# Kernel optimization log

Hardware: AMD Instinct MI355X
Metric: run time of the kernel (lower is better)

## Reference

```python
import jax, jax.numpy as jnp
import numpy as np

NUM_CLASSES = 80
CONF_THRESH = 0.05
NMS_THRESH = 0.6
TOPK = 1000
LEVEL_HWS = [40000, 10000, 2500, 640, 160]
CLASS_OFFSET = 2.0  # > max box coordinate so different classes never overlap (class-aware NMS)


def setup_inputs() -> dict:
    key = jax.random.key(0)
    inp = {}
    for i, hw in enumerate(LEVEL_HWS):
        k1, k2, k3, key = jax.random.split(key, 4)
        inp[f"cls_p{i + 3}"] = jax.random.normal(k1, (1, hw, NUM_CLASSES), jnp.float32)
        inp[f"ctn_p{i + 3}"] = jax.random.normal(k2, (1, hw, 1), jnp.float32)
        inp[f"box_p{i + 3}"] = jax.random.uniform(k3, (1, hw, 4), jnp.float32)
    inp["img_size"] = 1600
    return inp


def _level_select(cls_p, ctn_p, box_p):
    # cls_p: [1, HW, C], ctn_p: [1, HW, 1], box_p: [1, HW, 4]
    cls_p, ctn_p, box_p = cls_p[0], ctn_p[0], box_p[0]
    k = min(TOPK, box_p.shape[0])  # matches min(self.topk, box_pred_i.size(0))
    scores = jnp.sqrt(jax.nn.sigmoid(cls_p) * jax.nn.sigmoid(ctn_p)).reshape(-1)  # [HW*C]
    topk_scores, topk_idxs = jax.lax.top_k(scores, k)  # descending, == sort+slice
    valid = topk_scores > CONF_THRESH  # mask instead of dynamic filter (jit-friendly)
    labels = topk_idxs % NUM_CLASSES
    anchor_idxs = topk_idxs // NUM_CLASSES
    return topk_scores * valid, labels, box_p[anchor_idxs], valid


def _pairwise_iou(boxes):
    # boxes: [N, 4] xyxy
    x1, y1, x2, y2 = boxes[:, 0], boxes[:, 1], boxes[:, 2], boxes[:, 3]
    area = jnp.maximum(x2 - x1, 0.0) * jnp.maximum(y2 - y1, 0.0)
    ix1 = jnp.maximum(x1[:, None], x1[None, :])
    iy1 = jnp.maximum(y1[:, None], y1[None, :])
    ix2 = jnp.minimum(x2[:, None], x2[None, :])
    iy2 = jnp.minimum(y2[:, None], y2[None, :])
    inter = jnp.maximum(ix2 - ix1, 0.0) * jnp.maximum(iy2 - iy1, 0.0)
    union = area[:, None] + area[None, :] - inter
    return inter / jnp.maximum(union, 1e-9)


def _greedy_nms(scores, boxes, valid, thresh):
    # exact greedy NMS over a fixed-size candidate set; returns keep mask [N]
    n = scores.shape[0]
    order = jnp.argsort(-scores)
    iou = _pairwise_iou(boxes[order])  # [N, N]
    idx = jnp.arange(n)

    def body(i, keep):
        sup = (iou[i] > thresh) & keep[i] & (idx > i)
        return keep & (~sup)

    keep_o = jax.lax.fori_loop(0, n, body, valid[order])
    return jnp.zeros(n, dtype=bool).at[order].set(keep_o)


def reference(cls_p3, ctn_p3, box_p3, cls_p4, ctn_p4, box_p4,
              cls_p5, ctn_p5, box_p5, cls_p6, ctn_p6, box_p6,
              cls_p7, ctn_p7, box_p7, img_size):
    levels = [(cls_p3, ctn_p3, box_p3), (cls_p4, ctn_p4, box_p4),
              (cls_p5, ctn_p5, box_p5), (cls_p6, ctn_p6, box_p6),
              (cls_p7, ctn_p7, box_p7)]
    parts = [_level_select(c, t, b) for (c, t, b) in levels]
    scores = jnp.concatenate([p[0] for p in parts])   # [3800]
    labels = jnp.concatenate([p[1] for p in parts])   # [3800] int
    bboxes = jnp.concatenate([p[2] for p in parts])   # [3800, 4]
    valid = jnp.concatenate([p[3] for p in parts])    # [3800] bool
    # class-aware multiclass NMS via coordinate offset per class
    boxes_off = bboxes + (labels.astype(bboxes.dtype) * CLASS_OFFSET)[:, None]
    keep = _greedy_nms(jax.lax.stop_gradient(scores),
                       jax.lax.stop_gradient(boxes_off), valid, NMS_THRESH)
    # normalize to [0,1] by image size (square image: W == H == img_size)
    bboxes_n = jnp.clip(bboxes / jnp.float32(img_size), 0.0, 1.0)
    return scores * keep, labels, bboxes_n, keep
```

## Files before the change

kernel.cpp:

```cpp
#include <hip/hip_runtime.h>
#include <math.h>

#pragma clang fp contract(off)

typedef unsigned long long ull;

#define NCLS 80
#define NTOT 3800
#define CAND_CAP 4096
#define NMS_CAP 1024
#define CLS_CAP 128
#define BIN_LO 0x3F000000u
#define NB 1024
#define BSHIFT 13
#define QPB 1024
#define NBLK 1044
#define SEGCAP 320
#define ZWORDS 6496

__constant__ int d_BSQ[6]  = {0, 782, 978, 1027, 1040, 1044};
__constant__ int d_QL[5]   = {800000, 200000, 50000, 12800, 3200};
__constant__ int d_EL[5]   = {3200000, 800000, 200000, 51200, 12800};
__constant__ float d_PREHI[5] = {0.86f, 0.82f, 0.78f, 0.74f, 0.74f};
__constant__ int d_KL[5] = {1000,1000,1000,640,160};
__constant__ int d_OB[5] = {0,1000,2000,3000,3640};

struct Params {
  const float *cls0,*cls1,*cls2,*cls3,*cls4;
  const float *ctn0,*ctn1,*ctn2,*ctn3,*ctn4;
  const float *box0,*box1,*box2,*box3,*box4;
  const int* img;
  ull* pre;
  unsigned* tot;
  unsigned* ccount;
  unsigned* clscnt;
  unsigned* lvlbad;
  unsigned* blkcnt;
  ull* ckey;
  ull* clskey;
  unsigned* slot_bits;
  unsigned* slot_label;
  float* slot_box;
  float* out;
};

__device__ __forceinline__ float fast_sig(float x) {
  return 1.0f / (1.0f + __expf(-x));
}
__device__ __forceinline__ float fast_score(float c, float t) {
  return sqrtf(fast_sig(c) * fast_sig(t));
}
__device__ __forceinline__ float sigmoid_ref(float x) {
  float e = (float)exp(-(double)x);
  return 1.0f / (1.0f + e);
}
__device__ __forceinline__ float score_ref(float c, float t) {
  return sqrtf(sigmoid_ref(c) * sigmoid_ref(t));
}
__device__ __forceinline__ float iou_ref(float ax1,float ay1,float ax2,float ay2,
                                         float bx1,float by1,float bx2,float by2) {
  float areaA = fmaxf(ax2-ax1,0.0f) * fmaxf(ay2-ay1,0.0f);
  float areaB = fmaxf(bx2-bx1,0.0f) * fmaxf(by2-by1,0.0f);
  float ix1 = fmaxf(ax1,bx1), iy1 = fmaxf(ay1,by1);
  float ix2 = fminf(ax2,bx2), iy2 = fminf(ay2,by2);
  float inter = fmaxf(ix2-ix1,0.0f) * fmaxf(iy2-iy1,0.0f);
  float uni = areaA + areaB - inter;
  return inter / fmaxf(uni, 1e-9f);
}
__device__ __forceinline__ const float* cls_of(const Params& p, int l) {
  return (l==0)?p.cls0:(l==1)?p.cls1:(l==2)?p.cls2:(l==3)?p.cls3:p.cls4;
}
__device__ __forceinline__ const float* ctn_of(const Params& p, int l) {
  return (l==0)?p.ctn0:(l==1)?p.ctn1:(l==2)?p.ctn2:(l==3)?p.ctn3:p.ctn4;
}
__device__ __forceinline__ const float* box_of(const Params& p, int l) {
  return (l==0)?p.box0:(l==1)?p.box1:(l==2)?p.box2:(l==3)?p.box3:p.box4;
}

__global__ __launch_bounds__(256) void k_zero(unsigned* z) {
  for (int i = blockIdx.x*256 + threadIdx.x; i < ZWORDS; i += 256) z[i] = 0u;
}

__global__ __launch_bounds__(256) void k_score(Params p) {
  int b = blockIdx.x, tid = threadIdx.x;
  __shared__ unsigned h[NB];
  __shared__ ull pbuf[SEGCAP];
  __shared__ unsigned pcnt;
  for (int i = tid; i < NB; i += 256) h[i] = 0u;
  if (tid == 0) pcnt = 0u;
  __syncthreads();
  int l = 0;
  while (b >= d_BSQ[l+1]) ++l;
  int cb = b - d_BSQ[l];
  int q0 = cb * QPB;
  int nq = d_QL[l] - q0; if (nq > QPB) nq = QPB;
  const float* cls = cls_of(p, l);
  const float* ctn = ctn_of(p, l);
  float prehi = d_PREHI[l];
  for (int i = tid; i < nq; i += 256) {
    int q = q0 + i;
    float4 c4 = ((const float4*)cls)[q];
    float st = fast_sig(ctn[q / 20]);
    float s[4];
    s[0] = sqrtf(fast_sig(c4.x) * st);
    s[1] = sqrtf(fast_sig(c4.y) * st);
    s[2] = sqrtf(fast_sig(c4.z) * st);
    s[3] = sqrtf(fast_sig(c4.w) * st);
    #pragma unroll
    for (int j = 0; j < 4; ++j) {
      unsigned bits = __float_as_uint(s[j]);
      if (bits >= BIN_LO) atomicAdd(&h[(bits - BIN_LO) >> BSHIFT], 1u);
      if (s[j] >= prehi) {
        unsigned pos = atomicAdd(&pcnt, 1u);
        if (pos < SEGCAP)
          pbuf[pos] = ((ull)bits << 32) | (ull)(0xFFFFFFFFu - (unsigned)(4*q + j));
      }
    }
  }
  __syncthreads();
  unsigned* tl = p.tot + l*NB;
  for (int i = tid; i < NB; i += 256) {
    unsigned v = h[i];
    if (v) atomicAdd(&tl[i], v);
  }
  unsigned n = pcnt;
  if (tid == 0) {
    p.blkcnt[b] = n;
    if (n > SEGCAP) p.lvlbad[l] = 1u;
  }
  unsigned nw = n < SEGCAP ? n : SEGCAP;
  ull* seg = p.pre + (size_t)b * SEGCAP;
  for (unsigned i = tid; i < nw; i += 256) seg[i] = pbuf[i];
}

__global__ __launch_bounds__(256) void k_gather(Params p) {
  int bx = blockIdx.x;
  int l = bx >> 3, slice = bx & 7;
  int tid = threadIdx.x;
  __shared__ unsigned sfx[NB];
  __shared__ ull cbuf[CAND_CAP];
  __shared__ unsigned pcnt;
  __shared__ unsigned thr_sh;
  __shared__ unsigned base_sh;
  if (tid == 0) { pcnt = 0u; thr_sh = BIN_LO; }
  for (int j = tid; j < NB; j += 256) sfx[j] = p.tot[l*NB + j];
  __syncthreads();
  for (int off = 1; off < NB; off <<= 1) {
    unsigned v[4];
    #pragma unroll
    for (int j = 0; j < 4; ++j) {
      int idx = tid + j*256;
      unsigned add = (idx + off < NB) ? sfx[idx + off] : 0u;
      v[j] = sfx[idx] + add;
    }
    __syncthreads();
    #pragma unroll
    for (int j = 0; j < 4; ++j) sfx[tid + j*256] = v[j];
    __syncthreads();
  }
  unsigned k = (unsigned)d_KL[l];
  #pragma unroll
  for (int j = 0; j < 4; ++j) {
    int b = tid + j*256;
    unsigned s0 = sfx[b];
    unsigned s1 = (b + 1 < NB) ? sfx[b+1] : 0u;
    if (s0 >= k && (b == NB-1 || s1 < k)) {
      thr_sh = (b > 0) ? (BIN_LO + ((unsigned)(b-1) << BSHIFT)) : BIN_LO;
    }
  }
  __syncthreads();
  unsigned thr = thr_sh;
  const float* cls = cls_of(p, l);
  const float* ctn = ctn_of(p, l);
  bool fallback = (p.lvlbad[l] != 0u) || (thr < __float_as_uint(d_PREHI[l]));
  if (!fallback) {
    int s0b = d_BSQ[l], nseg = d_BSQ[l+1] - s0b;
    int chunk = (nseg + 7) >> 3;
    int sA = slice * chunk, sB = sA + chunk;
    if (sA > nseg) sA = nseg;
    if (sB > nseg) sB = nseg;
    int total = (sB - sA) * SEGCAP;
    const ull* base = p.pre + (size_t)(s0b + sA) * SEGCAP;
    const unsigned* bc = p.blkcnt + s0b + sA;
    for (int i = tid; i < total; i += 256) {
      int s = i / SEGCAP;
      int j = i - s * SEGCAP;
      unsigned cnt = bc[s]; if (cnt > SEGCAP) cnt = SEGCAP;
      if (j < (int)cnt) {
        ull kk = base[(size_t)s * SEGCAP + j];
        if ((unsigned)(kk >> 32) >= thr) {
          unsigned fi = 0xFFFFFFFFu - (unsigned)kk;
          float ex = score_ref(cls[fi], ctn[fi / NCLS]);
          unsigned pos = atomicAdd(&pcnt, 1u);
          if (pos < CAND_CAP)
            cbuf[pos] = ((ull)__float_as_uint(ex) << 32) | (ull)(0xFFFFFFFFu - fi);
        }
      }
    }
  } else {
    int ne = d_EL[l];
    int chunk = (ne + 7) >> 3;
    int eA = slice * chunk, eB = eA + chunk;
    if (eA > ne) eA = ne;
    if (eB > ne) eB = ne;
    for (int e = eA + tid; e < eB; e += 256) {
      float s = fast_score(cls[e], ctn[e / NCLS]);
      if (__float_as_uint(s) >= thr) {
        float ex = score_ref(cls[e], ctn[e / NCLS]);
        unsigned pos = atomicAdd(&pcnt, 1u);
        if (pos < CAND_CAP)
          cbuf[pos] = ((ull)__float_as_uint(ex) << 32) | (ull)(0xFFFFFFFFu - (unsigned)e);
      }
    }
  }
  __syncthreads();
  unsigned n = pcnt; if (n > CAND_CAP) n = CAND_CAP;
  if (tid == 0) base_sh = atomicAdd(&p.ccount[l*16], n);
  __syncthreads();
  unsigned bp = base_sh;
  ull* ck = p.ckey + (size_t)l * CAND_CAP;
  for (unsigned i = tid; i < n; i += 256) {
    unsigned d = bp + i;
    if (d < CAND_CAP) ck[d] = cbuf[i];
  }
}

__global__ __launch_bounds__(64) void k_rank(Params p) {
  int bx = blockIdx.x;
  int l = bx >> 6, slice = bx & 63;
  int tid = threadIdx.x;
  int m = (int)p.ccount[l*16]; if (m > CAND_CAP) m = CAND_CAP;
  int kL = d_KL[l], obase = d_OB[l];
  int i0 = slice * 64;
  int i = i0 + tid;
  if (i0 >= m) {
    if (i >= m && i < kL) {
      int g = obase + i;
      p.out[g] = 0.0f;
      p.out[NTOT + g] = 0.0f;
      ((float4*)(p.out + 2*NTOT))[g] = make_float4(0,0,0,0);
      p.out[6*NTOT + g] = 0.0f;
      ((float4*)p.slot_box)[g] = make_float4(0,0,0,0);
      p.slot_bits[g] = 0u;
      p.slot_label[g] = 0xFFFFFFFFu;
    }
    return;
  }
  __shared__ ull key[CAND_CAP];
  const ull* ck = p.ckey + (size_t)l * CAND_CAP;
  for (int j = tid; j < m; j += 64) key[j] = ck[j];
  __syncthreads();
  if (i >= m) {
    if (i < kL) {
      int g = obase + i;
      p.out[g] = 0.0f;
      p.out[NTOT + g] = 0.0f;
      ((float4*)(p.out + 2*NTOT))[g] = make_float4(0,0,0,0);
      p.out[6*NTOT + g] = 0.0f;
      ((float4*)p.slot_box)[g] = make_float4(0,0,0,0);
      p.slot_bits[g] = 0u;
      p.slot_label[g] = 0xFFFFFFFFu;
    }
    return;
  }
  ull mine = key[i];
  int rank = 0;
  int mm = m & ~7;
  #pragma unroll 1
  for (int j = 0; j < mm; j += 8) {
    rank += (key[j  ] > mine) + (key[j+1] > mine) + (key[j+2] > mine) + (key[j+3] > mine)
          + (key[j+4] > mine) + (key[j+5] > mine) + (key[j+6] > mine) + (key[j+7] > mine);
  }
  for (int j = mm; j < m; ++j) rank += (key[j] > mine) ? 1 : 0;
  if (rank >= kL) return;
  int g = obase + rank;
  unsigned bits = (unsigned)(mine >> 32);
  unsigned fi = 0xFFFFFFFFu - (unsigned)(mine & 0xFFFFFFFFu);
  unsigned lab = fi % NCLS;
  unsigned a = fi / NCLS;
  float img = (float)(*p.img);
  float4 b4 = ((const float4*)box_of(p, l))[a];
  float4 nb;
  nb.x = fminf(fmaxf(b4.x / img, 0.0f), 1.0f);
  nb.y = fminf(fmaxf(b4.y / img, 0.0f), 1.0f);
  nb.z = fminf(fmaxf(b4.z / img, 0.0f), 1.0f);
  nb.w = fminf(fmaxf(b4.w / img, 0.0f), 1.0f);
  p.out[NTOT + g] = (float)lab;
  ((float4*)(p.out + 2*NTOT))[g] = nb;
  ((float4*)p.slot_box)[g] = b4;
  p.slot_bits[g] = bits;
  p.slot_label[g] = lab;
  unsigned pos = atomicAdd(&p.clscnt[lab*16], 1u);
  if (pos < CLS_CAP)
    p.clskey[lab*CLS_CAP + pos] = ((ull)bits << 32) | (ull)(0xFFFFFFFFu - (unsigned)g);
}

__global__ __launch_bounds__(64) void k_nms(Params p) {
  int c = blockIdx.x, lane = threadIdx.x;
  int mc = (int)p.clscnt[c*16];
  if (mc == 0) return;
  if (mc <= 64) {
    ull kk = (lane < mc) ? p.clskey[c*CLS_CAP + lane] : 0ULL;
    int rank = 0;
    #pragma unroll 1
    for (int j = 0; j < 64; ++j) {
      ull kj = __shfl(kk, j);
      rank += (j < mc && kj > kk) ? 1 : 0;
    }
    __shared__ ull wkey[64];
    if (lane < mc) wkey[rank] = kk;
    __syncthreads();
    ull sk = (lane < mc) ? wkey[lane] : 0ULL;
    unsigned g = 0xFFFFFFFFu - (unsigned)(sk & 0xFFFFFFFFu);
    float s = __uint_as_float((unsigned)(sk >> 32));
    float off = 2.0f * (float)c;
    float x1=0,y1=0,x2=0,y2=0;
    if (lane < mc) {
      float4 b4 = ((const float4*)p.slot_box)[g];
      x1 = b4.x + off; y1 = b4.y + off; x2 = b4.z + off; y2 = b4.w + off;
    }
    ull keepm = __ballot(lane < mc && s > 0.05f);
    for (int i = 0; i + 1 < mc; ++i) {
      if ((keepm >> i) & 1ULL) {
        float ax1 = __shfl(x1, i), ay1 = __shfl(y1, i);
        float ax2 = __shfl(x2, i), ay2 = __shfl(y2, i);
        bool kept = (keepm >> lane) & 1ULL;
        bool sup = kept && (lane > i) && (lane < mc) &&
                   (iou_ref(ax1,ay1,ax2,ay2, x1,y1,x2,y2) > 0.6f);
        keepm &= ~__ballot(sup);
      }
    }
    if (lane < mc) {
      int kp = (int)((keepm >> lane) & 1ULL);
      p.out[g] = kp ? s : 0.0f;
      p.out[6*NTOT + g] = kp ? 1.0f : 0.0f;
    }
    return;
  }
  __shared__ ull key[NMS_CAP];
  __shared__ ull skey[NMS_CAP];
  __shared__ float bxs[NMS_CAP*4];
  __shared__ int keep[NMS_CAP];
  __shared__ unsigned mcnt_s;
  int m;
  if (mc <= CLS_CAP) {
    for (int j = lane; j < mc; j += 64) key[j] = p.clskey[c*CLS_CAP + j];
    m = mc;
    __syncthreads();
  } else {
    if (lane == 0) mcnt_s = 0u;
    __syncthreads();
    for (int g = lane; g < NTOT; g += 64) {
      if (p.slot_label[g] == (unsigned)c) {
        unsigned pos = atomicAdd(&mcnt_s, 1u);
        if (pos < NMS_CAP)
          key[pos] = ((ull)p.slot_bits[g] << 32) | (ull)(0xFFFFFFFFu - (unsigned)g);
      }
    }
    __syncthreads();
    m = (mcnt_s < NMS_CAP) ? (int)mcnt_s : NMS_CAP;
  }
  for (int i = lane; i < m; i += 64) {
    ull mine = key[i];
    int rank = 0;
    for (int j = 0; j < m; ++j) rank += (key[j] > mine) ? 1 : 0;
    skey[rank] = mine;
  }
  __syncthreads();
  float off = 2.0f * (float)c;
  for (int j = lane; j < m; j += 64) {
    ull kk = skey[j];
    unsigned g = 0xFFFFFFFFu - (unsigned)(kk & 0xFFFFFFFFu);
    for (int q = 0; q < 4; ++q) bxs[j*4+q] = p.slot_box[g*4+q] + off;
    float s = __uint_as_float((unsigned)(kk >> 32));
    keep[j] = (s > 0.05f) ? 1 : 0;
  }
  __syncthreads();
  for (int i = 0; i + 1 < m; ++i) {
    if (keep[i]) {
      float ax1 = bxs[i*4+0], ay1 = bxs[i*4+1], ax2 = bxs[i*4+2], ay2 = bxs[i*4+3];
      for (int j = i + 1 + lane; j < m; j += 64) {
        if (keep[j]) {
          if (iou_ref(ax1,ay1,ax2,ay2, bxs[j*4+0],bxs[j*4+1],bxs[j*4+2],bxs[j*4+3]) > 0.6f)
            keep[j] = 0;
        }
      }
    }
    __syncthreads();
  }
  for (int j = lane; j < m; j += 64) {
    ull kk = skey[j];
    unsigned g = 0xFFFFFFFFu - (unsigned)(kk & 0xFFFFFFFFu);
    float s = __uint_as_float((unsigned)(kk >> 32));
    int kp = keep[j];
    p.out[g] = kp ? s : 0.0f;
    p.out[6*NTOT + g] = kp ? 1.0f : 0.0f;
  }
}

extern "C" void kernel_launch(void* const* d_in, const int* in_sizes, int n_in,
                              void* d_out, int out_size, void* d_ws, size_t ws_size,
                              hipStream_t stream) {
  Params p;
  p.cls0 = (const float*)d_in[0];  p.ctn0 = (const float*)d_in[1];  p.box0 = (const float*)d_in[2];
  p.cls1 = (const float*)d_in[3];  p.ctn1 = (const float*)d_in[4];  p.box1 = (const float*)d_in[5];
  p.cls2 = (const float*)d_in[6];  p.ctn2 = (const float*)d_in[7];  p.box2 = (const float*)d_in[8];
  p.cls3 = (const float*)d_in[9];  p.ctn3 = (const float*)d_in[10]; p.box3 = (const float*)d_in[11];
  p.cls4 = (const float*)d_in[12]; p.ctn4 = (const float*)d_in[13]; p.box4 = (const float*)d_in[14];
  p.img  = (const int*)d_in[15];

  char* w = (char*)d_ws;
  p.pre = (ull*)w;            w += (size_t)NBLK*SEGCAP*8;
  unsigned* zbase = (unsigned*)w;
  p.tot    = zbase;
  p.ccount = zbase + 5120;
  p.clscnt = zbase + 5120 + 80;
  p.lvlbad = zbase + 5120 + 80 + 1280;
  w += (size_t)ZWORDS*4;
  p.blkcnt = (unsigned*)w;    w += (size_t)NBLK*4 + 64;
  p.ckey = (ull*)w;           w += (size_t)5*CAND_CAP*8;
  p.clskey = (ull*)w;         w += (size_t)NCLS*CLS_CAP*8;
  p.slot_bits  = (unsigned*)w; w += NTOT*4;
  p.slot_label = (unsigned*)w; w += NTOT*4;
  p.slot_box   = (float*)w;    w += NTOT*16;
  p.out = (float*)d_out;

  hipLaunchKernelGGL(k_zero,   dim3(1),     dim3(256), 0, stream, zbase);
  hipLaunchKernelGGL(k_score,  dim3(NBLK),  dim3(256), 0, stream, p);
  hipLaunchKernelGGL(k_gather, dim3(40),    dim3(256), 0, stream, p);
  hipLaunchKernelGGL(k_rank,   dim3(5*64),  dim3(64),  0, stream, p);
  hipLaunchKernelGGL(k_nms,    dim3(80),    dim3(64),  0, stream, p);
}
```

Baseline: 209.5 us.

## Fuse gather into score and rank kernels, compacting candidates globally

```diff
diff --git a/kernel.cpp b/kernel.cpp
--- a/kernel.cpp
+++ b/kernel.cpp
@@ -15,7 +15,8 @@
 #define BSHIFT 13
 #define QPB 1024
 #define NBLK 1044
-#define SEGCAP 320
+#define PBUF_CAP 320
+#define GCAP 16384
 #define ZWORDS 6496
 
 __constant__ int d_BSQ[6]  = {0, 782, 978, 1027, 1040, 1044};
@@ -30,13 +31,11 @@
   const float *ctn0,*ctn1,*ctn2,*ctn3,*ctn4;
   const float *box0,*box1,*box2,*box3,*box4;
   const int* img;
-  ull* pre;
   unsigned* tot;
-  unsigned* ccount;
+  unsigned* gcnt;
   unsigned* clscnt;
   unsigned* lvlbad;
-  unsigned* blkcnt;
-  ull* ckey;
+  ull* gcand;
   ull* clskey;
   unsigned* slot_bits;
   unsigned* slot_label;
@@ -83,10 +82,9 @@
 
 __global__ __launch_bounds__(256) void k_score(Params p) {
   int b = blockIdx.x, tid = threadIdx.x;
-  __shared__ unsigned h[NB];
-  __shared__ ull pbuf[SEGCAP];
+  __shared__ ull pbuf[PBUF_CAP];
   __shared__ unsigned pcnt;
-  for (int i = tid; i < NB; i += 256) h[i] = 0u;
+  __shared__ unsigned base_sh;
   if (tid == 0) pcnt = 0u;
   __syncthreads();
   int l = 0;
@@ -97,159 +95,122 @@
   const float* cls = cls_of(p, l);
   const float* ctn = ctn_of(p, l);
   float prehi = d_PREHI[l];
+  unsigned* tl = p.tot + l*NB;
   for (int i = tid; i < nq; i += 256) {
     int q = q0 + i;
     float4 c4 = ((const float4*)cls)[q];
-    float st = fast_sig(ctn[q / 20]);
-    float s[4];
-    s[0] = sqrtf(fast_sig(c4.x) * st);
-    s[1] = sqrtf(fast_sig(c4.y) * st);
-    s[2] = sqrtf(fast_sig(c4.z) * st);
-    s[3] = sqrtf(fast_sig(c4.w) * st);
+    float ct = ctn[q / 20];
+    float st = fast_sig(ct);
+    float cv[4] = {c4.x, c4.y, c4.z, c4.w};
     #pragma unroll
     for (int j = 0; j < 4; ++j) {
-      unsigned bits = __float_as_uint(s[j]);
-      if (bits >= BIN_LO) atomicAdd(&h[(bits - BIN_LO) >> BSHIFT], 1u);
-      if (s[j] >= prehi) {
+      float s = sqrtf(fast_sig(cv[j]) * st);
+      if (s >= prehi) {
+        unsigned fb = __float_as_uint(s);
+        unsigned bin = (fb - BIN_LO) >> BSHIFT;
+        if (bin > NB-1) bin = NB-1;
+        atomicAdd(&tl[bin], 1u);
+        float ex = score_ref(cv[j], ct);
         unsigned pos = atomicAdd(&pcnt, 1u);
-        if (pos < SEGCAP)
-          pbuf[pos] = ((ull)bits << 32) | (ull)(0xFFFFFFFFu - (unsigned)(4*q + j));
-      }
-    }
-  }
-  __syncthreads();
-  unsigned* tl = p.tot + l*NB;
-  for (int i = tid; i < NB; i += 256) {
-    unsigned v = h[i];
-    if (v) atomicAdd(&tl[i], v);
-  }
+        if (pos < PBUF_CAP)
+          pbuf[pos] = ((ull)__float_as_uint(ex) << 32)
+                    | (ull)(0xFFFFFFFFu - (unsigned)(4*q + j));
+      }
+    }
+  }
+  __syncthreads();
   unsigned n = pcnt;
-  if (tid == 0) {
-    p.blkcnt[b] = n;
-    if (n > SEGCAP) p.lvlbad[l] = 1u;
-  }
-  unsigned nw = n < SEGCAP ? n : SEGCAP;
-  ull* seg = p.pre + (size_t)b * SEGCAP;
-  for (unsigned i = tid; i < nw; i += 256) seg[i] = pbuf[i];
-}
-
-__global__ __launch_bounds__(256) void k_gather(Params p) {
-  int bx = blockIdx.x;
-  int l = bx >> 3, slice = bx & 7;
-  int tid = threadIdx.x;
-  __shared__ unsigned sfx[NB];
-  __shared__ ull cbuf[CAND_CAP];
-  __shared__ unsigned pcnt;
-  __shared__ unsigned thr_sh;
-  __shared__ unsigned base_sh;
-  if (tid == 0) { pcnt = 0u; thr_sh = BIN_LO; }
-  for (int j = tid; j < NB; j += 256) sfx[j] = p.tot[l*NB + j];
-  __syncthreads();
-  for (int off = 1; off < NB; off <<= 1) {
-    unsigned v[4];
-    #pragma unroll
-    for (int j = 0; j < 4; ++j) {
-      int idx = tid + j*256;
-      unsigned add = (idx + off < NB) ? sfx[idx + off] : 0u;
-      v[j] = sfx[idx] + add;
-    }
-    __syncthreads();
-    #pragma unroll
-    for (int j = 0; j < 4; ++j) sfx[tid + j*256] = v[j];
-    __syncthreads();
-  }
-  unsigned k = (unsigned)d_KL[l];
-  #pragma unroll
-  for (int j = 0; j < 4; ++j) {
-    int b = tid + j*256;
-    unsigned s0 = sfx[b];
-    unsigned s1 = (b + 1 < NB) ? sfx[b+1] : 0u;
-    if (s0 >= k && (b == NB-1 || s1 < k)) {
-      thr_sh = (b > 0) ? (BIN_LO + ((unsigned)(b-1) << BSHIFT)) : BIN_LO;
-    }
-  }
-  __syncthreads();
-  unsigned thr = thr_sh;
-  const float* cls = cls_of(p, l);
-  const float* ctn = ctn_of(p, l);
-  bool fallback = (p.lvlbad[l] != 0u) || (thr < __float_as_uint(d_PREHI[l]));
-  if (!fallback) {
-    int s0b = d_BSQ[l], nseg = d_BSQ[l+1] - s0b;
-    int chunk = (nseg + 7) >> 3;
-    int sA = slice * chunk, sB = sA + chunk;
-    if (sA > nseg) sA = nseg;
-    if (sB > nseg) sB = nseg;
-    int total = (sB - sA) * SEGCAP;
-    const ull* base = p.pre + (size_t)(s0b + sA) * SEGCAP;
-    const unsigned* bc = p.blkcnt + s0b + sA;
-    for (int i = tid; i < total; i += 256) {
-      int s = i / SEGCAP;
-      int j = i - s * SEGCAP;
-      unsigned cnt = bc[s]; if (cnt > SEGCAP) cnt = SEGCAP;
-      if (j < (int)cnt) {
-        ull kk = base[(size_t)s * SEGCAP + j];
-        if ((unsigned)(kk >> 32) >= thr) {
-          unsigned fi = 0xFFFFFFFFu - (unsigned)kk;
-          float ex = score_ref(cls[fi], ctn[fi / NCLS]);
-          unsigned pos = atomicAdd(&pcnt, 1u);
-          if (pos < CAND_CAP)
-            cbuf[pos] = ((ull)__float_as_uint(ex) << 32) | (ull)(0xFFFFFFFFu - fi);
-        }
-      }
-    }
-  } else {
-    int ne = d_EL[l];
-    int chunk = (ne + 7) >> 3;
-    int eA = slice * chunk, eB = eA + chunk;
-    if (eA > ne) eA = ne;
-    if (eB > ne) eB = ne;
-    for (int e = eA + tid; e < eB; e += 256) {
-      float s = fast_score(cls[e], ctn[e / NCLS]);
-      if (__float_as_uint(s) >= thr) {
-        float ex = score_ref(cls[e], ctn[e / NCLS]);
-        unsigned pos = atomicAdd(&pcnt, 1u);
-        if (pos < CAND_CAP)
-          cbuf[pos] = ((ull)__float_as_uint(ex) << 32) | (ull)(0xFFFFFFFFu - (unsigned)e);
-      }
-    }
-  }
-  __syncthreads();
-  unsigned n = pcnt; if (n > CAND_CAP) n = CAND_CAP;
-  if (tid == 0) base_sh = atomicAdd(&p.ccount[l*16], n);
-  __syncthreads();
-  unsigned bp = base_sh;
-  ull* ck = p.ckey + (size_t)l * CAND_CAP;
+  if (n > PBUF_CAP) { if (tid == 0) p.lvlbad[l] = 1u; n = PBUF_CAP; }
+  if (tid == 0) base_sh = atomicAdd(&p.gcnt[l*16], n);
+  __syncthreads();
+  unsigned base = base_sh;
+  ull* gc = p.gcand + (size_t)l * GCAP;
   for (unsigned i = tid; i < n; i += 256) {
-    unsigned d = bp + i;
-    if (d < CAND_CAP) ck[d] = cbuf[i];
+    unsigned d = base + i;
+    if (d < GCAP) gc[d] = pbuf[i];
+    else p.lvlbad[l] = 1u;
   }
 }
 
 __global__ __launch_bounds__(64) void k_rank(Params p) {
   int bx = blockIdx.x;
   int l = bx >> 6, slice = bx & 63;
-  int tid = threadIdx.x;
-  int m = (int)p.ccount[l*16]; if (m > CAND_CAP) m = CAND_CAP;
+  int lane = threadIdx.x;
+  __shared__ unsigned hist[NB];
+  __shared__ ull key[CAND_CAP];
+  for (int j = 0; j < NB/64; ++j)
+    hist[lane + j*64] = p.tot[l*NB + lane + j*64];
+  __syncthreads();
+  int chunkbase = 1008 - 16*lane;
+  unsigned csum = 0;
+  #pragma unroll
+  for (int t = 0; t < 16; ++t) csum += hist[chunkbase + t];
+  unsigned cum = csum;
+  for (int d = 1; d < 64; d <<= 1) {
+    unsigned tu = __shfl_up(cum, d);
+    if (lane >= d) cum += tu;
+  }
+  unsigned k = (unsigned)d_KL[l];
+  ull okm = __ballot(cum >= k);
+  unsigned thr = BIN_LO;
+  if (okm) {
+    int j0 = (int)__ffsll((long long)okm) - 1;
+    if (lane == j0) {
+      unsigned acc = cum - csum;
+      int cb2 = 1008 - 16*j0;
+      for (int bb = cb2 + 15; bb >= cb2; --bb) {
+        acc += hist[bb];
+        if (acc >= k) {
+          if (bb > 0) thr = BIN_LO + ((unsigned)(bb - 1) << BSHIFT);
+          break;
+        }
+      }
+    }
+    thr = __shfl(thr, j0);
+  }
+  bool fastok = (p.lvlbad[l] == 0u) && (thr >= __float_as_uint(d_PREHI[l]));
+  int m = 0;
+  if (fastok) {
+    int gn = (int)p.gcnt[l*16]; if (gn > GCAP) gn = GCAP;
+    const ull* gc = p.gcand + (size_t)l * GCAP;
+    for (int i0 = 0; i0 < gn; i0 += 64) {
+      int i = i0 + lane;
+      ull kk = (i < gn) ? gc[i] : 0ULL;
+      bool pred = (i < gn) && ((unsigned)(kk >> 32) >= thr);
+      ull mask = __ballot(pred);
+      if (pred) {
+        int pos = m + (int)__popcll(mask & ((1ULL << lane) - 1ULL));
+        if (pos < CAND_CAP) key[pos] = kk;
+      }
+      m += (int)__popcll(mask);
+    }
+  } else {
+    int ne = d_EL[l];
+    const float* cls = cls_of(p, l);
+    const float* ctn = ctn_of(p, l);
+    for (int i0 = 0; i0 < ne; i0 += 64) {
+      int i = i0 + lane;
+      bool pred = false; ull kk = 0ULL;
+      if (i < ne) {
+        float fs = fast_score(cls[i], ctn[i / NCLS]);
+        if (__float_as_uint(fs) >= thr) {
+          float ex = score_ref(cls[i], ctn[i / NCLS]);
+          kk = ((ull)__float_as_uint(ex) << 32) | (ull)(0xFFFFFFFFu - (unsigned)i);
+          pred = true;
+        }
+      }
+      ull mask = __ballot(pred);
+      if (pred) {
+        int pos = m + (int)__popcll(mask & ((1ULL << lane) - 1ULL));
+        if (pos < CAND_CAP) key[pos] = kk;
+      }
+      m += (int)__popcll(mask);
+    }
+  }
+  if (m > CAND_CAP) m = CAND_CAP;
+  __syncthreads();
   int kL = d_KL[l], obase = d_OB[l];
-  int i0 = slice * 64;
-  int i = i0 + tid;
-  if (i0 >= m) {
-    if (i >= m && i < kL) {
-      int g = obase + i;
-      p.out[g] = 0.0f;
-      p.out[NTOT + g] = 0.0f;
-      ((float4*)(p.out + 2*NTOT))[g] = make_float4(0,0,0,0);
-      p.out[6*NTOT + g] = 0.0f;
-      ((float4*)p.slot_box)[g] = make_float4(0,0,0,0);
-      p.slot_bits[g] = 0u;
-      p.slot_label[g] = 0xFFFFFFFFu;
-    }
-    return;
-  }
-  __shared__ ull key[CAND_CAP];
-  const ull* ck = p.ckey + (size_t)l * CAND_CAP;
-  for (int j = tid; j < m; j += 64) key[j] = ck[j];
-  __syncthreads();
+  int i = slice*64 + lane;
   if (i >= m) {
     if (i < kL) {
       int g = obase + i;
@@ -410,24 +371,21 @@
   p.img  = (const int*)d_in[15];
 
   char* w = (char*)d_ws;
-  p.pre = (ull*)w;            w += (size_t)NBLK*SEGCAP*8;
   unsigned* zbase = (unsigned*)w;
   p.tot    = zbase;
-  p.ccount = zbase + 5120;
+  p.gcnt   = zbase + 5120;
   p.clscnt = zbase + 5120 + 80;
   p.lvlbad = zbase + 5120 + 80 + 1280;
   w += (size_t)ZWORDS*4;
-  p.blkcnt = (unsigned*)w;    w += (size_t)NBLK*4 + 64;
-  p.ckey = (ull*)w;           w += (size_t)5*CAND_CAP*8;
-  p.clskey = (ull*)w;         w += (size_t)NCLS*CLS_CAP*8;
+  p.gcand = (ull*)w;           w += (size_t)5*GCAP*8;
+  p.clskey = (ull*)w;          w += (size_t)NCLS*CLS_CAP*8;
   p.slot_bits  = (unsigned*)w; w += NTOT*4;
   p.slot_label = (unsigned*)w; w += NTOT*4;
   p.slot_box   = (float*)w;    w += NTOT*16;
   p.out = (float*)d_out;
 
-  hipLaunchKernelGGL(k_zero,   dim3(1),     dim3(256), 0, stream, zbase);
-  hipLaunchKernelGGL(k_score,  dim3(NBLK),  dim3(256), 0, stream, p);
-  hipLaunchKernelGGL(k_gather, dim3(40),    dim3(256), 0, stream, p);
-  hipLaunchKernelGGL(k_rank,   dim3(5*64),  dim3(64),  0, stream, p);
-  hipLaunchKernelGGL(k_nms,    dim3(80),    dim3(64),  0, stream, p);
-}
+  hipLaunchKernelGGL(k_zero,  dim3(1),    dim3(256), 0, stream, zbase);
+  hipLaunchKernelGGL(k_score, dim3(NBLK), dim3(256), 0, stream, p);
+  hipLaunchKernelGGL(k_rank,  dim3(5*64), dim3(64),  0, stream, p);
+  hipLaunchKernelGGL(k_nms,   dim3(80),   dim3(64),  0, stream, p);
+}
```

Measured after the change: 527.0 us. 152% more time.

## Compact pre-candidates globally and compute exact scores in the scoring kernel

Applied to the files above, without the earlier changes.

```diff
diff --git a/kernel.cpp b/kernel.cpp
--- a/kernel.cpp
+++ b/kernel.cpp
@@ -15,8 +15,9 @@
 #define BSHIFT 13
 #define QPB 1024
 #define NBLK 1044
-#define SEGCAP 320
-#define ZWORDS 6496
+#define PBUF_CAP 320
+#define GCAP 65536
+#define ZWORDS 6576
 
 __constant__ int d_BSQ[6]  = {0, 782, 978, 1027, 1040, 1044};
 __constant__ int d_QL[5]   = {800000, 200000, 50000, 12800, 3200};
@@ -30,12 +31,12 @@
   const float *ctn0,*ctn1,*ctn2,*ctn3,*ctn4;
   const float *box0,*box1,*box2,*box3,*box4;
   const int* img;
-  ull* pre;
   unsigned* tot;
+  unsigned* gcnt;
   unsigned* ccount;
   unsigned* clscnt;
   unsigned* lvlbad;
-  unsigned* blkcnt;
+  ull* gcand;
   ull* ckey;
   ull* clskey;
   unsigned* slot_bits;
@@ -83,10 +84,9 @@
 
 __global__ __launch_bounds__(256) void k_score(Params p) {
   int b = blockIdx.x, tid = threadIdx.x;
-  __shared__ unsigned h[NB];
-  __shared__ ull pbuf[SEGCAP];
+  __shared__ ull pbuf[PBUF_CAP];
   __shared__ unsigned pcnt;
-  for (int i = tid; i < NB; i += 256) h[i] = 0u;
+  __shared__ unsigned base_sh;
   if (tid == 0) pcnt = 0u;
   __syncthreads();
   int l = 0;
@@ -97,43 +97,44 @@
   const float* cls = cls_of(p, l);
   const float* ctn = ctn_of(p, l);
   float prehi = d_PREHI[l];
+  unsigned* tl = p.tot + l*NB;
   for (int i = tid; i < nq; i += 256) {
     int q = q0 + i;
     float4 c4 = ((const float4*)cls)[q];
-    float st = fast_sig(ctn[q / 20]);
-    float s[4];
-    s[0] = sqrtf(fast_sig(c4.x) * st);
-    s[1] = sqrtf(fast_sig(c4.y) * st);
-    s[2] = sqrtf(fast_sig(c4.z) * st);
-    s[3] = sqrtf(fast_sig(c4.w) * st);
+    float ct = ctn[q / 20];
+    float st = fast_sig(ct);
+    float cv[4] = {c4.x, c4.y, c4.z, c4.w};
     #pragma unroll
     for (int j = 0; j < 4; ++j) {
-      unsigned bits = __float_as_uint(s[j]);
-      if (bits >= BIN_LO) atomicAdd(&h[(bits - BIN_LO) >> BSHIFT], 1u);
-      if (s[j] >= prehi) {
+      float s = sqrtf(fast_sig(cv[j]) * st);
+      if (s >= prehi) {
+        unsigned fb = __float_as_uint(s);
+        unsigned bin = (fb - BIN_LO) >> BSHIFT;
+        if (bin > NB-1) bin = NB-1;
+        atomicAdd(&tl[bin], 1u);
+        float ex = score_ref(cv[j], ct);
         unsigned pos = atomicAdd(&pcnt, 1u);
-        if (pos < SEGCAP)
-          pbuf[pos] = ((ull)bits << 32) | (ull)(0xFFFFFFFFu - (unsigned)(4*q + j));
-      }
-    }
-  }
-  __syncthreads();
-  unsigned* tl = p.tot + l*NB;
-  for (int i = tid; i < NB; i += 256) {
-    unsigned v = h[i];
-    if (v) atomicAdd(&tl[i], v);
-  }
+        if (pos < PBUF_CAP)
+          pbuf[pos] = ((ull)__float_as_uint(ex) << 32)
+                    | (ull)(0xFFFFFFFFu - (unsigned)(4*q + j));
+      }
+    }
+  }
+  __syncthreads();
   unsigned n = pcnt;
-  if (tid == 0) {
-    p.blkcnt[b] = n;
-    if (n > SEGCAP) p.lvlbad[l] = 1u;
-  }
-  unsigned nw = n < SEGCAP ? n : SEGCAP;
-  ull* seg = p.pre + (size_t)b * SEGCAP;
-  for (unsigned i = tid; i < nw; i += 256) seg[i] = pbuf[i];
-}
-
-__global__ __launch_bounds__(256) void k_gather(Params p) {
+  if (n > PBUF_CAP) { if (tid == 0) p.lvlbad[l] = 1u; n = PBUF_CAP; }
+  if (tid == 0) base_sh = atomicAdd(&p.gcnt[l*16], n);
+  __syncthreads();
+  unsigned base = base_sh;
+  ull* gc = p.gcand + (size_t)l * GCAP;
+  for (unsigned i = tid; i < n; i += 256) {
+    unsigned d = base + i;
+    if (d < GCAP) gc[d] = pbuf[i];
+    else p.lvlbad[l] = 1u;
+  }
+}
+
+__global__ __launch_bounds__(256) void k_filter(Params p) {
   int bx = blockIdx.x;
   int l = bx >> 3, slice = bx & 7;
   int tid = threadIdx.x;
@@ -164,37 +165,26 @@
     int b = tid + j*256;
     unsigned s0 = sfx[b];
     unsigned s1 = (b + 1 < NB) ? sfx[b+1] : 0u;
-    if (s0 >= k && (b == NB-1 || s1 < k)) {
+    if (s0 >= k && (b == NB-1 || s1 < k))
       thr_sh = (b > 0) ? (BIN_LO + ((unsigned)(b-1) << BSHIFT)) : BIN_LO;
-    }
   }
   __syncthreads();
   unsigned thr = thr_sh;
   const float* cls = cls_of(p, l);
   const float* ctn = ctn_of(p, l);
-  bool fallback = (p.lvlbad[l] != 0u) || (thr < __float_as_uint(d_PREHI[l]));
-  if (!fallback) {
-    int s0b = d_BSQ[l], nseg = d_BSQ[l+1] - s0b;
-    int chunk = (nseg + 7) >> 3;
-    int sA = slice * chunk, sB = sA + chunk;
-    if (sA > nseg) sA = nseg;
-    if (sB > nseg) sB = nseg;
-    int total = (sB - sA) * SEGCAP;
-    const ull* base = p.pre + (size_t)(s0b + sA) * SEGCAP;
-    const unsigned* bc = p.blkcnt + s0b + sA;
-    for (int i = tid; i < total; i += 256) {
-      int s = i / SEGCAP;
-      int j = i - s * SEGCAP;
-      unsigned cnt = bc[s]; if (cnt > SEGCAP) cnt = SEGCAP;
-      if (j < (int)cnt) {
-        ull kk = base[(size_t)s * SEGCAP + j];
-        if ((unsigned)(kk >> 32) >= thr) {
-          unsigned fi = 0xFFFFFFFFu - (unsigned)kk;
-          float ex = score_ref(cls[fi], ctn[fi / NCLS]);
-          unsigned pos = atomicAdd(&pcnt, 1u);
-          if (pos < CAND_CAP)
-            cbuf[pos] = ((ull)__float_as_uint(ex) << 32) | (ull)(0xFFFFFFFFu - fi);
-        }
+  bool fastok = (p.lvlbad[l] == 0u) && (thr >= __float_as_uint(d_PREHI[l]));
+  if (fastok) {
+    int gn = (int)p.gcnt[l*16]; if (gn > GCAP) gn = GCAP;
+    int chunk = (gn + 7) >> 3;
+    int iA = slice * chunk, iB = iA + chunk;
+    if (iA > gn) iA = gn;
+    if (iB > gn) iB = gn;
+    const ull* gc = p.gcand + (size_t)l * GCAP;
+    for (int i = iA + tid; i < iB; i += 256) {
+      ull kk = gc[i];
+      if ((unsigned)(kk >> 32) >= thr) {
+        unsigned pos = atomicAdd(&pcnt, 1u);
+        if (pos < CAND_CAP) cbuf[pos] = kk;
       }
     }
   } else {
@@ -204,12 +194,13 @@
     if (eA > ne) eA = ne;
     if (eB > ne) eB = ne;
     for (int e = eA + tid; e < eB; e += 256) {
-      float s = fast_score(cls[e], ctn[e / NCLS]);
-      if (__float_as_uint(s) >= thr) {
+      float fs = fast_score(cls[e], ctn[e / NCLS]);
+      if (__float_as_uint(fs) >= thr) {
         float ex = score_ref(cls[e], ctn[e / NCLS]);
         unsigned pos = atomicAdd(&pcnt, 1u);
         if (pos < CAND_CAP)
-          cbuf[pos] = ((ull)__float_as_uint(ex) << 32) | (ull)(0xFFFFFFFFu - (unsigned)e);
+          cbuf[pos] = ((ull)__float_as_uint(ex) << 32)
+                    | (ull)(0xFFFFFFFFu - (unsigned)e);
       }
     }
   }
@@ -228,12 +219,11 @@
 __global__ __launch_bounds__(64) void k_rank(Params p) {
   int bx = blockIdx.x;
   int l = bx >> 6, slice = bx & 63;
-  int tid = threadIdx.x;
+  int lane = threadIdx.x;
   int m = (int)p.ccount[l*16]; if (m > CAND_CAP) m = CAND_CAP;
   int kL = d_KL[l], obase = d_OB[l];
-  int i0 = slice * 64;
-  int i = i0 + tid;
-  if (i0 >= m) {
+  int i = slice*64 + lane;
+  if (slice*64 >= m) {
     if (i >= m && i < kL) {
       int g = obase + i;
       p.out[g] = 0.0f;
@@ -248,7 +238,7 @@
   }
   __shared__ ull key[CAND_CAP];
   const ull* ck = p.ckey + (size_t)l * CAND_CAP;
-  for (int j = tid; j < m; j += 64) key[j] = ck[j];
+  for (int j = lane; j < m; j += 64) key[j] = ck[j];
   __syncthreads();
   if (i >= m) {
     if (i < kL) {
@@ -410,24 +400,24 @@
   p.img  = (const int*)d_in[15];
 
   char* w = (char*)d_ws;
-  p.pre = (ull*)w;            w += (size_t)NBLK*SEGCAP*8;
   unsigned* zbase = (unsigned*)w;
   p.tot    = zbase;
-  p.ccount = zbase + 5120;
-  p.clscnt = zbase + 5120 + 80;
-  p.lvlbad = zbase + 5120 + 80 + 1280;
+  p.gcnt   = zbase + 5120;
+  p.ccount = zbase + 5120 + 80;
+  p.clscnt = zbase + 5120 + 160;
+  p.lvlbad = zbase + 5120 + 160 + 1280;
   w += (size_t)ZWORDS*4;
-  p.blkcnt = (unsigned*)w;    w += (size_t)NBLK*4 + 64;
-  p.ckey = (ull*)w;           w += (size_t)5*CAND_CAP*8;
-  p.clskey = (ull*)w;         w += (size_t)NCLS*CLS_CAP*8;
+  p.gcand = (ull*)w;           w += (size_t)5*GCAP*8;
+  p.ckey  = (ull*)w;           w += (size_t)5*CAND_CAP*8;
+  p.clskey = (ull*)w;          w += (size_t)NCLS*CLS_CAP*8;
   p.slot_bits  = (unsigned*)w; w += NTOT*4;
   p.slot_label = (unsigned*)w; w += NTOT*4;
   p.slot_box   = (float*)w;    w += NTOT*16;
   p.out = (float*)d_out;
 
-  hipLaunchKernelGGL(k_zero,   dim3(1),     dim3(256), 0, stream, zbase);
-  hipLaunchKernelGGL(k_score,  dim3(NBLK),  dim3(256), 0, stream, p);
-  hipLaunchKernelGGL(k_gather, dim3(40),    dim3(256), 0, stream, p);
-  hipLaunchKernelGGL(k_rank,   dim3(5*64),  dim3(64),  0, stream, p);
-  hipLaunchKernelGGL(k_nms,    dim3(80),    dim3(64),  0, stream, p);
-}
+  hipLaunchKernelGGL(k_zero,   dim3(1),    dim3(256), 0, stream, zbase);
+  hipLaunchKernelGGL(k_score,  dim3(NBLK), dim3(256), 0, stream, p);
+  hipLaunchKernelGGL(k_filter, dim3(40),   dim3(256), 0, stream, p);
+  hipLaunchKernelGGL(k_rank,   dim3(5*64), dim3(64),  0, stream, p);
+  hipLaunchKernelGGL(k_nms,    dim3(80),   dim3(64),  0, stream, p);
+}
```

Result: faster. 187.5 us (-10.5%).
